# Optimization experiments

Measured on AMD Instinct MI355X. Metric: run time of the kernel, lower is better.

Reference implementation:

```python
import jax, jax.numpy as jnp
import numpy as np

N_NODES = 50000
ELU_ALPHA = 0.2  # torch.nn.ELU(0.2): alpha=0.2


def _elu(v, alpha):
    return jnp.where(v > 0, v, alpha * jnp.expm1(v))


def setup_inputs() -> dict:
    key = jax.random.key(0)
    k1, k2, k3, k4, k5 = jax.random.split(key, 5)
    fin, H, F = 128, 4, 32
    E = 1600000
    return {
        "x": jax.random.normal(k1, (N_NODES, fin), dtype=jnp.float32),
        "W": jax.random.normal(k2, (fin, H * F), dtype=jnp.float32) * (1.414 / np.sqrt(fin)),
        "a_src": jax.random.normal(k3, (H, F), dtype=jnp.float32) * 0.1,
        "a_tgt": jax.random.normal(k4, (H, F), dtype=jnp.float32) * 0.1,
        "edge_index": jax.random.randint(k5, (E, 2), 0, N_NODES, dtype=jnp.int64),
    }


def reference(x, W, a_src, a_tgt, edge_index):
    # GAT layer (dropout omitted: eval mode). x: [N, fin]
    N = x.shape[0]
    H, F = a_src.shape
    xp = (x @ W).reshape(N, H, F)                 # projected node feats [N,H,F]
    s_src = jnp.einsum("nhf,hf->nh", xp, a_src)   # per-head source scores [N,H]
    s_tgt = jnp.einsum("nhf,hf->nh", xp, a_tgt)   # per-head target scores [N,H]

    src = edge_index[:, 0]
    tgt = edge_index[:, 1]

    # edge-wise gather (the memory-bound hotspot)
    e = _elu(s_src[src] + s_tgt[tgt], ELU_ALPHA)  # [E,H]

    # segment softmax over edges sharing a target node
    m = jax.ops.segment_max(e, tgt, num_segments=N)           # [N,H]
    m = jnp.where(jnp.isfinite(m), m, 0.0)
    ex = jnp.exp(e - m[tgt])                                  # [E,H]
    denom = jax.ops.segment_sum(ex, tgt, num_segments=N)      # [N,H]
    alpha = ex / denom[tgt]                                   # [E,H]

    # gather source features, weight, scatter-add into target nodes
    msg = alpha[:, :, None] * xp[src]                          # [E,H,F]
    out = jax.ops.segment_sum(msg, tgt, num_segments=N)        # [N,H,F]
    return out.reshape(N, H * F)                               # concat heads
```

## Files before the change

### kernel.cpp

```cpp
#include <hip/hip_runtime.h>
#include <hip/hip_bf16.h>
#include <math.h>

#define FIN 128
#define NHEAD 4
#define CH 128
#define ELU_A 0.2f

#define BSHIFT 8
#define NB 196
#define CAP 16384
#define T_EDGES 2048

typedef unsigned int uint32;
typedef __attribute__((ext_vector_type(8))) short short8;
typedef __attribute__((ext_vector_type(4))) float f32x4;

__device__ __forceinline__ float bf16lo(uint32 u) {
    union { uint32 i; float f; } c; c.i = u << 16; return c.f;
}
__device__ __forceinline__ float bf16hi(uint32 u) {
    union { uint32 i; float f; } c; c.i = u & 0xffff0000u; return c.f;
}
__device__ __forceinline__ unsigned short f2b(float f) {
    union { float f; uint32 u; } c; c.f = f;
    uint32 u = c.u;
    return (unsigned short)((u + 0x7fffu + ((u >> 16) & 1u)) >> 16);
}

__global__ __launch_bounds__(256) void wprep_kernel(
    const float* __restrict__ W, unsigned short* __restrict__ Wt)
{
    __shared__ float w[FIN * CH];
    for (int i = threadIdx.x; i < FIN * CH; i += 256) w[i] = W[i];
    __syncthreads();
    const int n  = threadIdx.x >> 1;
    const int kh = (threadIdx.x & 1) * 64;
    for (int kb = 0; kb < 64; kb += 8) {
        unsigned short v[8];
#pragma unroll
        for (int j = 0; j < 8; ++j) v[j] = f2b(w[(kh + kb + j) * CH + n]);
        *(uint4*)&Wt[(size_t)n * FIN + kh + kb] = *(uint4*)v;
    }
}

__global__ __launch_bounds__(256) void gemm_mfma_kernel(
    const float* __restrict__ x, const unsigned short* __restrict__ Wt,
    unsigned short* __restrict__ xpb, int N)
{
    __shared__ unsigned short cbuf[4][16][132];
    const int lane = threadIdx.x & 63;
    const int wid  = threadIdx.x >> 6;
    const int rowbase = blockIdx.x * 64 + wid * 16;

    const int rr   = min(rowbase + (lane & 15), N - 1);
    const int krow = (lane >> 4) * 8;

    f32x4 acc[8];
#pragma unroll
    for (int c = 0; c < 8; ++c) acc[c] = (f32x4){0.f, 0.f, 0.f, 0.f};

#pragma unroll
    for (int s = 0; s < 4; ++s) {
        const int koff = s * 32 + krow;
        const float* xr = x + (size_t)rr * FIN + koff;
        float4 p0 = *(const float4*)xr;
        float4 p1 = *(const float4*)(xr + 4);
        short8 af;
        af[0] = (short)f2b(p0.x); af[1] = (short)f2b(p0.y);
        af[2] = (short)f2b(p0.z); af[3] = (short)f2b(p0.w);
        af[4] = (short)f2b(p1.x); af[5] = (short)f2b(p1.y);
        af[6] = (short)f2b(p1.z); af[7] = (short)f2b(p1.w);
#pragma unroll
        for (int c = 0; c < 8; ++c) {
            const short8 bf = *(const short8*)&Wt[(size_t)(c * 16 + (lane & 15)) * FIN + koff];
            acc[c] = __builtin_amdgcn_mfma_f32_16x16x32_bf16(af, bf, acc[c], 0, 0, 0);
        }
    }

#pragma unroll
    for (int c = 0; c < 8; ++c)
#pragma unroll
        for (int r = 0; r < 4; ++r)
            cbuf[wid][(lane >> 4) * 4 + r][c * 16 + (lane & 15)] = f2b(acc[c][r]);
    __syncthreads();

    for (int r = 0; r < 16; ++r) {
        int row = rowbase + r;
        if (row < N) {
            uint32 v = *(const uint32*)&cbuf[wid][r][lane * 2];
            *(uint32*)&xpb[(size_t)row * CH + lane * 2] = v;
        }
    }
}

__global__ __launch_bounds__(256) void scores_kernel(
    const uint32* __restrict__ xpb, const float* __restrict__ a_src,
    const float* __restrict__ a_tgt, float* __restrict__ s_src,
    float* __restrict__ s_tgt, int N)
{
    const int t = threadIdx.x;
    const int n = blockIdx.x * 16 + (t >> 4);
    const int g = t & 15;
    if (n >= N) return;

    uint4 xv = *(const uint4*)&xpb[(size_t)n * 64 + g * 4];
    float xs[8] = { bf16lo(xv.x), bf16hi(xv.x), bf16lo(xv.y), bf16hi(xv.y),
                    bf16lo(xv.z), bf16hi(xv.z), bf16lo(xv.w), bf16hi(xv.w) };
    float4 as0 = *(const float4*)&a_src[g * 8];
    float4 as1 = *(const float4*)&a_src[g * 8 + 4];
    float4 at0 = *(const float4*)&a_tgt[g * 8];
    float4 at1 = *(const float4*)&a_tgt[g * 8 + 4];

    float ps = xs[0]*as0.x + xs[1]*as0.y + xs[2]*as0.z + xs[3]*as0.w
             + xs[4]*as1.x + xs[5]*as1.y + xs[6]*as1.z + xs[7]*as1.w;
    float pt = xs[0]*at0.x + xs[1]*at0.y + xs[2]*at0.z + xs[3]*at0.w
             + xs[4]*at1.x + xs[5]*at1.y + xs[6]*at1.z + xs[7]*at1.w;

    ps += __shfl_xor(ps, 1); ps += __shfl_xor(ps, 2);
    pt += __shfl_xor(pt, 1); pt += __shfl_xor(pt, 2);

    if ((g & 3) == 0) {
        int h = g >> 2;
        s_src[(size_t)n * NHEAD + h] = ps;
        s_tgt[(size_t)n * NHEAD + h] = pt;
    }
}

__global__ __launch_bounds__(256) void partition_kernel(
    const int2* __restrict__ ei2, int* __restrict__ bcnt,
    uint32* __restrict__ ebuck, int E)
{
    __shared__ uint32 stage[T_EDGES];
    __shared__ int hist[256], scanbuf[256], loff[256], cnt2[256], base[256];
    const int tid = threadIdx.x;
    const int e0 = blockIdx.x * T_EDGES;
    const int tile = min(T_EDGES, E - e0);

    hist[tid] = 0; cnt2[tid] = 0;
    __syncthreads();

    uint32 rec[8];
#pragma unroll
    for (int j = 0; j < 8; ++j) {
        int idx = e0 + j * 256 + tid;
        if (idx < E) {
            int2 p = ei2[idx];
            rec[j] = (uint32)p.x | ((uint32)p.y << 16);
            atomicAdd(&hist[p.y >> BSHIFT], 1);
        } else rec[j] = 0xFFFFFFFFu;
    }
    __syncthreads();

    scanbuf[tid] = hist[tid];
    __syncthreads();
    for (int off = 1; off < 256; off <<= 1) {
        int v = (tid >= off) ? scanbuf[tid - off] : 0;
        __syncthreads();
        scanbuf[tid] += v;
        __syncthreads();
    }
    loff[tid] = scanbuf[tid] - hist[tid];
    if (tid < NB && hist[tid] > 0)
        base[tid] = tid * CAP + atomicAdd(&bcnt[tid], hist[tid]);
    __syncthreads();

#pragma unroll
    for (int j = 0; j < 8; ++j) {
        if (rec[j] != 0xFFFFFFFFu) {
            int b = rec[j] >> (16 + BSHIFT);
            int r = atomicAdd(&cnt2[b], 1);
            stage[loff[b] + r] = rec[j];
        }
    }
    __syncthreads();

    for (int i = tid; i < tile; i += 256) {
        uint32 rc = stage[i];
        int b = rc >> (16 + BSHIFT);
        ebuck[(size_t)base[b] + (i - loff[b])] = rc;
    }
}

__global__ __launch_bounds__(256) void bscan_kernel(
    const int* __restrict__ bcnt, int* __restrict__ bbase)
{
    __shared__ int s[256];
    const int t = threadIdx.x;
    int v = (t < NB) ? bcnt[t] : 0;
    s[t] = v;
    __syncthreads();
    for (int off = 1; off < 256; off <<= 1) {
        int u = (t >= off) ? s[t - off] : 0;
        __syncthreads();
        s[t] += u;
        __syncthreads();
    }
    if (t < NB) bbase[t] = s[t] - v;
}

__global__ __launch_bounds__(1024) void fine_scatter_kernel(
    const uint32* __restrict__ ebuck, const int* __restrict__ bcnt,
    const int* __restrict__ bbase, int* __restrict__ deg,
    int* __restrict__ rowptr, int* __restrict__ srcs, int N)
{
    __shared__ int ldeg[256], psum[256], lcur[256];
    const int b = blockIdx.x;
    const int tid = threadIdx.x;
    if (tid < 256) ldeg[tid] = 0;
    __syncthreads();

    const int cnt = bcnt[b];
    const uint32* rp = ebuck + (size_t)b * CAP;

    for (int i = tid; i < cnt; i += 1024)
        atomicAdd(&ldeg[(rp[i] >> 16) & 255], 1);
    __syncthreads();

    if (tid < 256) psum[tid] = ldeg[tid];
    __syncthreads();
    for (int off = 1; off < 256; off <<= 1) {
        int u = 0;
        if (tid < 256 && tid >= off) u = psum[tid - off];
        __syncthreads();
        if (tid < 256) psum[tid] += u;
        __syncthreads();
    }

    const int gb = bbase[b];
    if (tid < 256) {
        int pref = gb + psum[tid] - ldeg[tid];
        lcur[tid] = pref;
        int node = b * 256 + tid;
        if (node < N) { deg[node] = ldeg[tid]; rowptr[node] = pref; }
    }
    __syncthreads();

    for (int i = tid; i < cnt; i += 1024) {
        uint32 rc = rp[i];
        int pos = atomicAdd(&lcur[(rc >> 16) & 255], 1);
        srcs[pos] = rc & 0xffff;
    }
}

__global__ __launch_bounds__(256) void aggregate_kernel(
    const int* __restrict__ srcs, const int* __restrict__ rowptr,
    const int* __restrict__ deg, const float* __restrict__ s_src,
    const float* __restrict__ s_tgt, const uint32* __restrict__ xpb,
    float* __restrict__ out, int N)
{
    const int lane = threadIdx.x & 63;
    const int wid  = __builtin_amdgcn_readfirstlane(threadIdx.x >> 6);
    const int t = blockIdx.x * 4 + wid;
    if (t >= N) return;

    const int start = __builtin_amdgcn_readfirstlane(rowptr[t]);
    const int d     = __builtin_amdgcn_readfirstlane(deg[t]);
    const int h     = lane >> 4;
    const int cj    = lane & 7;
    const int chh   = (lane >> 3) & 3;

    const float st_c = s_tgt[(size_t)t * NHEAD + chh];
    const float st_h = s_tgt[(size_t)t * NHEAD + h];
    const int bb = h * 8;

    float accx = 0.0f, accy = 0.0f, dsum = 0.0f;
    int k = 0;

    for (; k + 8 <= d; k += 8) {
        int   sv = srcs[start + k + cj];
        float a  = s_src[(size_t)sv * NHEAD + chh];
        float v  = a + st_c;
        float u  = v > 0.0f ? v : ELU_A * (__expf(v) - 1.0f);
        float e  = __expf(u);

        int s0 = srcs[start + k + 0], s1 = srcs[start + k + 1];
        int s2 = srcs[start + k + 2], s3 = srcs[start + k + 3];
        int s4 = srcs[start + k + 4], s5 = srcs[start + k + 5];
        int s6 = srcs[start + k + 6], s7 = srcs[start + k + 7];

        uint32 x0 = xpb[(size_t)s0 * 64 + lane];
        uint32 x1 = xpb[(size_t)s1 * 64 + lane];
        uint32 x2 = xpb[(size_t)s2 * 64 + lane];
        uint32 x3 = xpb[(size_t)s3 * 64 + lane];
        uint32 x4 = xpb[(size_t)s4 * 64 + lane];
        uint32 x5 = xpb[(size_t)s5 * 64 + lane];
        uint32 x6 = xpb[(size_t)s6 * 64 + lane];
        uint32 x7 = xpb[(size_t)s7 * 64 + lane];

        float e0 = __shfl(e, bb + 0), e1 = __shfl(e, bb + 1);
        float e2 = __shfl(e, bb + 2), e3 = __shfl(e, bb + 3);
        float e4 = __shfl(e, bb + 4), e5 = __shfl(e, bb + 5);
        float e6 = __shfl(e, bb + 6), e7 = __shfl(e, bb + 7);

#define ACC(E, X) { dsum += (E); accx += (E) * bf16lo(X); accy += (E) * bf16hi(X); }
        ACC(e0, x0) ACC(e1, x1) ACC(e2, x2) ACC(e3, x3)
        ACC(e4, x4) ACC(e5, x5) ACC(e6, x6) ACC(e7, x7)
#undef ACC
    }

    for (; k < d; ++k) {
        int   s  = srcs[start + k];
        float a  = s_src[(size_t)s * NHEAD + h];
        uint32 xv = xpb[(size_t)s * 64 + lane];
        float v = a + st_h;
        float u = v > 0.0f ? v : ELU_A * (__expf(v) - 1.0f);
        float e = __expf(u);
        dsum += e; accx += e * bf16lo(xv); accy += e * bf16hi(xv);
    }

    float inv = (d > 0) ? 1.0f / dsum : 0.0f;
    float2 o = make_float2(accx * inv, accy * inv);
    *(float2*)&out[(size_t)t * CH + lane * 2] = o;
}

extern "C" void kernel_launch(void* const* d_in, const int* in_sizes, int n_in,
                              void* d_out, int out_size, void* d_ws, size_t ws_size,
                              hipStream_t stream)
{
    const float* x     = (const float*)d_in[0];
    const float* W     = (const float*)d_in[1];
    const float* a_src = (const float*)d_in[2];
    const float* a_tgt = (const float*)d_in[3];
    const int*   ei    = (const int*)d_in[4];

    const int N = in_sizes[0] / FIN;
    const int E = in_sizes[4] / 2;

    char* ws = (char*)d_ws;
    unsigned short* xpb = (unsigned short*)ws;  ws += (size_t)N * CH * sizeof(unsigned short);
    unsigned short* Wt  = (unsigned short*)ws;  ws += (size_t)FIN * CH * sizeof(unsigned short);
    float* s_src  = (float*)ws;                 ws += (size_t)N * NHEAD * sizeof(float);
    float* s_tgt  = (float*)ws;                 ws += (size_t)N * NHEAD * sizeof(float);
    int*   deg    = (int*)ws;                   ws += (size_t)N * sizeof(int);
    int*   bcnt   = (int*)ws;                   ws += (size_t)NB * sizeof(int);
    int*   bbase  = (int*)ws;                   ws += (size_t)NB * sizeof(int);
    int*   rowptr = (int*)ws;                   ws += (size_t)N * sizeof(int);
    int*   srcs   = (int*)ws;                   ws += (size_t)E * sizeof(int);
    uint32* ebuck = (uint32*)ws;                ws += (size_t)NB * CAP * sizeof(uint32);

    float* out = (float*)d_out;
    const int2* ei2 = (const int2*)ei;

    hipMemsetAsync(bcnt, 0, (size_t)NB * sizeof(int), stream);

    wprep_kernel<<<1, 256, 0, stream>>>(W, Wt);
    partition_kernel<<<(E + T_EDGES - 1) / T_EDGES, 256, 0, stream>>>(
        ei2, bcnt, ebuck, E);
    bscan_kernel<<<1, 256, 0, stream>>>(bcnt, bbase);
    fine_scatter_kernel<<<NB, 1024, 0, stream>>>(
        ebuck, bcnt, bbase, deg, rowptr, srcs, N);

    gemm_mfma_kernel<<<(N + 63) / 64, 256, 0, stream>>>(x, Wt, xpb, N);
    scores_kernel<<<(N + 15) / 16, 256, 0, stream>>>(
        (const uint32*)xpb, a_src, a_tgt, s_src, s_tgt, N);

    aggregate_kernel<<<(N + 3) / 4, 256, 0, stream>>>(
        srcs, rowptr, deg, s_src, s_tgt, (const uint32*)xpb, out, N);
}
```

Before: 133.5 us.

## Fold W prep, bucket scan and score computation into partition and GEMM kernels

Weight transpose/bf16 conversion is moved into an extra last block of the partition kernel, and the bucket-offset scan becomes an extra last block of the GEMM kernel. Per-node attention scores are now computed from the GEMM's shared-memory output tile instead of a separate kernel that re-read xpb from global memory. This cuts the launch count from seven kernels to four and removes one pass over the projected features. The trade-off is extra divergent blocks inside the larger kernels and a little more work per GEMM block.

```diff
diff --git a/kernel.cpp b/kernel.cpp
--- a/kernel.cpp
+++ b/kernel.cpp
@@ -28,27 +28,99 @@
     return (unsigned short)((u + 0x7fffu + ((u >> 16) & 1u)) >> 16);
 }
 
-__global__ __launch_bounds__(256) void wprep_kernel(
-    const float* __restrict__ W, unsigned short* __restrict__ Wt)
-{
-    __shared__ float w[FIN * CH];
-    for (int i = threadIdx.x; i < FIN * CH; i += 256) w[i] = W[i];
-    __syncthreads();
-    const int n  = threadIdx.x >> 1;
-    const int kh = (threadIdx.x & 1) * 64;
-    for (int kb = 0; kb < 64; kb += 8) {
-        unsigned short v[8];
-#pragma unroll
-        for (int j = 0; j < 8; ++j) v[j] = f2b(w[(kh + kb + j) * CH + n]);
-        *(uint4*)&Wt[(size_t)n * FIN + kh + kb] = *(uint4*)v;
-    }
-}
-
-__global__ __launch_bounds__(256) void gemm_mfma_kernel(
+__global__ __launch_bounds__(256) void partition_kernel(
+    const int2* __restrict__ ei2, int* __restrict__ bcnt,
+    uint32* __restrict__ ebuck, const float* __restrict__ W,
+    unsigned short* __restrict__ Wt, int E)
+{
+    if (blockIdx.x == gridDim.x - 1) {
+        for (int task = threadIdx.x; task < CH * (FIN / 8); task += 256) {
+            int n  = task >> 4;
+            int k0 = (task & 15) * 8;
+            unsigned short v[8];
+#pragma unroll
+            for (int j = 0; j < 8; ++j) v[j] = f2b(W[(size_t)(k0 + j) * CH + n]);
+            *(uint4*)&Wt[(size_t)n * FIN + k0] = *(uint4*)v;
+        }
+        return;
+    }
+
+    __shared__ uint32 stage[T_EDGES];
+    __shared__ int hist[256], scanbuf[256], loff[256], cnt2[256], base[256];
+    const int tid = threadIdx.x;
+    const int e0 = blockIdx.x * T_EDGES;
+    const int tile = min(T_EDGES, E - e0);
+
+    hist[tid] = 0; cnt2[tid] = 0;
+    __syncthreads();
+
+    uint32 rec[8];
+#pragma unroll
+    for (int j = 0; j < 8; ++j) {
+        int idx = e0 + j * 256 + tid;
+        if (idx < E) {
+            int2 p = ei2[idx];
+            rec[j] = (uint32)p.x | ((uint32)p.y << 16);
+            atomicAdd(&hist[p.y >> BSHIFT], 1);
+        } else rec[j] = 0xFFFFFFFFu;
+    }
+    __syncthreads();
+
+    scanbuf[tid] = hist[tid];
+    __syncthreads();
+    for (int off = 1; off < 256; off <<= 1) {
+        int v = (tid >= off) ? scanbuf[tid - off] : 0;
+        __syncthreads();
+        scanbuf[tid] += v;
+        __syncthreads();
+    }
+    loff[tid] = scanbuf[tid] - hist[tid];
+    if (tid < NB && hist[tid] > 0)
+        base[tid] = tid * CAP + atomicAdd(&bcnt[tid], hist[tid]);
+    __syncthreads();
+
+#pragma unroll
+    for (int j = 0; j < 8; ++j) {
+        if (rec[j] != 0xFFFFFFFFu) {
+            int b = rec[j] >> (16 + BSHIFT);
+            int r = atomicAdd(&cnt2[b], 1);
+            stage[loff[b] + r] = rec[j];
+        }
+    }
+    __syncthreads();
+
+    for (int i = tid; i < tile; i += 256) {
+        uint32 rc = stage[i];
+        int b = rc >> (16 + BSHIFT);
+        ebuck[(size_t)base[b] + (i - loff[b])] = rc;
+    }
+}
+
+__global__ __launch_bounds__(256) void gemm_bscan_kernel(
     const float* __restrict__ x, const unsigned short* __restrict__ Wt,
-    unsigned short* __restrict__ xpb, int N)
+    unsigned short* __restrict__ xpb, const float* __restrict__ a_src,
+    const float* __restrict__ a_tgt, float* __restrict__ s_src,
+    float* __restrict__ s_tgt, const int* __restrict__ bcnt,
+    int* __restrict__ bbase, int N)
 {
     __shared__ unsigned short cbuf[4][16][132];
+
+    if (blockIdx.x == gridDim.x - 1) {
+        int* s = (int*)&cbuf[0][0][0];
+        const int t = threadIdx.x;
+        int v = (t < NB) ? bcnt[t] : 0;
+        s[t] = v;
+        __syncthreads();
+        for (int off = 1; off < 256; off <<= 1) {
+            int u = (t >= off) ? s[t - off] : 0;
+            __syncthreads();
+            s[t] += u;
+            __syncthreads();
+        }
+        if (t < NB) bbase[t] = s[t] - v;
+        return;
+    }
+
     const int lane = threadIdx.x & 63;
     const int wid  = threadIdx.x >> 6;
     const int rowbase = blockIdx.x * 64 + wid * 16;
@@ -92,111 +164,36 @@
             *(uint32*)&xpb[(size_t)row * CH + lane * 2] = v;
         }
     }
-}
-
-__global__ __launch_bounds__(256) void scores_kernel(
-    const uint32* __restrict__ xpb, const float* __restrict__ a_src,
-    const float* __restrict__ a_tgt, float* __restrict__ s_src,
-    float* __restrict__ s_tgt, int N)
-{
-    const int t = threadIdx.x;
-    const int n = blockIdx.x * 16 + (t >> 4);
-    const int g = t & 15;
-    if (n >= N) return;
-
-    uint4 xv = *(const uint4*)&xpb[(size_t)n * 64 + g * 4];
-    float xs[8] = { bf16lo(xv.x), bf16hi(xv.x), bf16lo(xv.y), bf16hi(xv.y),
-                    bf16lo(xv.z), bf16hi(xv.z), bf16lo(xv.w), bf16hi(xv.w) };
-    float4 as0 = *(const float4*)&a_src[g * 8];
-    float4 as1 = *(const float4*)&a_src[g * 8 + 4];
-    float4 at0 = *(const float4*)&a_tgt[g * 8];
-    float4 at1 = *(const float4*)&a_tgt[g * 8 + 4];
-
-    float ps = xs[0]*as0.x + xs[1]*as0.y + xs[2]*as0.z + xs[3]*as0.w
-             + xs[4]*as1.x + xs[5]*as1.y + xs[6]*as1.z + xs[7]*as1.w;
-    float pt = xs[0]*at0.x + xs[1]*at0.y + xs[2]*at0.z + xs[3]*at0.w
-             + xs[4]*at1.x + xs[5]*at1.y + xs[6]*at1.z + xs[7]*at1.w;
-
-    ps += __shfl_xor(ps, 1); ps += __shfl_xor(ps, 2);
-    pt += __shfl_xor(pt, 1); pt += __shfl_xor(pt, 2);
-
-    if ((g & 3) == 0) {
-        int h = g >> 2;
-        s_src[(size_t)n * NHEAD + h] = ps;
-        s_tgt[(size_t)n * NHEAD + h] = pt;
-    }
-}
-
-__global__ __launch_bounds__(256) void partition_kernel(
-    const int2* __restrict__ ei2, int* __restrict__ bcnt,
-    uint32* __restrict__ ebuck, int E)
-{
-    __shared__ uint32 stage[T_EDGES];
-    __shared__ int hist[256], scanbuf[256], loff[256], cnt2[256], base[256];
-    const int tid = threadIdx.x;
-    const int e0 = blockIdx.x * T_EDGES;
-    const int tile = min(T_EDGES, E - e0);
-
-    hist[tid] = 0; cnt2[tid] = 0;
-    __syncthreads();
-
-    uint32 rec[8];
-#pragma unroll
-    for (int j = 0; j < 8; ++j) {
-        int idx = e0 + j * 256 + tid;
-        if (idx < E) {
-            int2 p = ei2[idx];
-            rec[j] = (uint32)p.x | ((uint32)p.y << 16);
-            atomicAdd(&hist[p.y >> BSHIFT], 1);
-        } else rec[j] = 0xFFFFFFFFu;
-    }
-    __syncthreads();
-
-    scanbuf[tid] = hist[tid];
-    __syncthreads();
-    for (int off = 1; off < 256; off <<= 1) {
-        int v = (tid >= off) ? scanbuf[tid - off] : 0;
-        __syncthreads();
-        scanbuf[tid] += v;
-        __syncthreads();
-    }
-    loff[tid] = scanbuf[tid] - hist[tid];
-    if (tid < NB && hist[tid] > 0)
-        base[tid] = tid * CAP + atomicAdd(&bcnt[tid], hist[tid]);
-    __syncthreads();
-
-#pragma unroll
-    for (int j = 0; j < 8; ++j) {
-        if (rec[j] != 0xFFFFFFFFu) {
-            int b = rec[j] >> (16 + BSHIFT);
-            int r = atomicAdd(&cnt2[b], 1);
-            stage[loff[b] + r] = rec[j];
-        }
-    }
-    __syncthreads();
-
-    for (int i = tid; i < tile; i += 256) {
-        uint32 rc = stage[i];
-        int b = rc >> (16 + BSHIFT);
-        ebuck[(size_t)base[b] + (i - loff[b])] = rc;
-    }
-}
-
-__global__ __launch_bounds__(256) void bscan_kernel(
-    const int* __restrict__ bcnt, int* __restrict__ bbase)
-{
-    __shared__ int s[256];
-    const int t = threadIdx.x;
-    int v = (t < NB) ? bcnt[t] : 0;
-    s[t] = v;
-    __syncthreads();
-    for (int off = 1; off < 256; off <<= 1) {
-        int u = (t >= off) ? s[t - off] : 0;
-        __syncthreads();
-        s[t] += u;
-        __syncthreads();
-    }
-    if (t < NB) bbase[t] = s[t] - v;
+
+    {
+        const int srow = lane >> 2;
+        const int sh   = lane & 3;
+        const unsigned short* cp = &cbuf[wid][srow][sh * 32];
+        const float* as = a_src + sh * 32;
+        const float* at = a_tgt + sh * 32;
+        float ps = 0.f, pt = 0.f;
+#pragma unroll
+        for (int q = 0; q < 4; ++q) {
+            uint4 u = *(const uint4*)&cp[q * 8];
+            float4 a0 = *(const float4*)&as[q * 8];
+            float4 a1 = *(const float4*)&as[q * 8 + 4];
+            float4 b0 = *(const float4*)&at[q * 8];
+            float4 b1 = *(const float4*)&at[q * 8 + 4];
+            float l0 = bf16lo(u.x), h0 = bf16hi(u.x);
+            float l1 = bf16lo(u.y), h1 = bf16hi(u.y);
+            float l2 = bf16lo(u.z), h2 = bf16hi(u.z);
+            float l3 = bf16lo(u.w), h3 = bf16hi(u.w);
+            ps += l0*a0.x + h0*a0.y + l1*a0.z + h1*a0.w
+                + l2*a1.x + h2*a1.y + l3*a1.z + h3*a1.w;
+            pt += l0*b0.x + h0*b0.y + l1*b0.z + h1*b0.w
+                + l2*b1.x + h2*b1.y + l3*b1.z + h3*b1.w;
+        }
+        int node = rowbase + srow;
+        if (node < N) {
+            s_src[(size_t)node * NHEAD + sh] = ps;
+            s_tgt[(size_t)node * NHEAD + sh] = pt;
+        }
+    }
 }
 
 __global__ __launch_bounds__(1024) void fine_scatter_kernel(
@@ -326,6 +323,8 @@
 
     const int N = in_sizes[0] / FIN;
     const int E = in_sizes[4] / 2;
+    const int PB = (E + T_EDGES - 1) / T_EDGES;
+    const int GB = (N + 63) / 64;
 
     char* ws = (char*)d_ws;
     unsigned short* xpb = (unsigned short*)ws;  ws += (size_t)N * CH * sizeof(unsigned short);
@@ -344,17 +343,11 @@
 
     hipMemsetAsync(bcnt, 0, (size_t)NB * sizeof(int), stream);
 
-    wprep_kernel<<<1, 256, 0, stream>>>(W, Wt);
-    partition_kernel<<<(E + T_EDGES - 1) / T_EDGES, 256, 0, stream>>>(
-        ei2, bcnt, ebuck, E);
-    bscan_kernel<<<1, 256, 0, stream>>>(bcnt, bbase);
+    partition_kernel<<<PB + 1, 256, 0, stream>>>(ei2, bcnt, ebuck, W, Wt, E);
+    gemm_bscan_kernel<<<GB + 1, 256, 0, stream>>>(
+        x, Wt, xpb, a_src, a_tgt, s_src, s_tgt, bcnt, bbase, N);
     fine_scatter_kernel<<<NB, 1024, 0, stream>>>(
         ebuck, bcnt, bbase, deg, rowptr, srcs, N);
-
-    gemm_mfma_kernel<<<(N + 63) / 64, 256, 0, stream>>>(x, Wt, xpb, N);
-    scores_kernel<<<(N + 15) / 16, 256, 0, stream>>>(
-        (const uint32*)xpb, a_src, a_tgt, s_src, s_tgt, N);
-
     aggregate_kernel<<<(N + 3) / 4, 256, 0, stream>>>(
         srcs, rowptr, deg, s_src, s_tgt, (const uint32*)xpb, out, N);
 }
```

After: 134.4 us. No clear change (+0.7%).
